# Kernel optimization log

Hardware: AMD Instinct MI355X
Metric: run time of the kernel (lower is better)

The kernel has to match this reference:

```python
import jax, jax.numpy as jnp
import numpy as np

B, N, M, DQ, DK, DV, H = 8, 1024, 1024, 512, 512, 512, 8
DS = DV // H  # dim_split = 64
NEG = -1e38


def _ln(x, g, b, eps=1e-5):
    mu = jnp.mean(x, -1, keepdims=True)
    var = jnp.mean((x - mu) ** 2, -1, keepdims=True)
    return (x - mu) * jax.lax.rsqrt(var + eps) * g + b


def setup_inputs() -> dict:
    key = jax.random.key(0)
    ks = jax.random.split(key, 16)
    s = 0.02
    return {
        "x": jax.random.normal(ks[0], (B, N, DQ), jnp.float32),
        "y": jax.random.normal(ks[1], (B, M, DK), jnp.float32),
        "x_mask": jax.random.randint(ks[2], (B, N), 0, 2).astype(bool),
        "y_mask": jax.random.randint(ks[3], (B, M), 0, 2).astype(bool),
        "Wq": jax.random.normal(ks[4], (DQ, DV), jnp.float32) * s,
        "Wk": jax.random.normal(ks[5], (DK, DV), jnp.float32) * s,
        "Wv": jax.random.normal(ks[6], (DK, DV), jnp.float32) * s,
        "Wo": jax.random.normal(ks[7], (DV, DQ), jnp.float32) * s,
        "W1": jax.random.normal(ks[8], (DQ, DQ), jnp.float32) * s,
        "b1": jnp.zeros((DQ,), jnp.float32),
        "W2": jax.random.normal(ks[9], (DQ, DQ), jnp.float32) * s,
        "b2": jnp.zeros((DQ,), jnp.float32),
        "g1": jnp.ones((DQ,), jnp.float32),
        "be1": jnp.zeros((DQ,), jnp.float32),
        "g2": jnp.ones((DQ,), jnp.float32),
        "be2": jnp.zeros((DQ,), jnp.float32),
    }


def reference(x, y, x_mask, y_mask, Wq, Wk, Wv, Wo, W1, b1, W2, b2, g1, be1, g2, be2):
    xm = x_mask[..., None]  # [B,N,1]
    ym = y_mask[..., None]  # [B,M,1]
    x = jnp.where(xm, 0.0, x)
    y = jnp.where(ym, 0.0, y)
    # projections (no bias); masked rows stay zero, re-mask as in source
    q = jnp.where(xm, 0.0, x @ Wq).reshape(B, N, H, DS)
    k = jnp.where(ym, 0.0, y @ Wk).reshape(B, M, H, DS)
    v = jnp.where(ym, 0.0, y @ Wv).reshape(B, M, H, DS)
    # scaled dot product; NOTE: scale is sqrt(dim_v), faithful to source
    sdp = jnp.einsum('bnhd,bmhd->bhnm', q, k) / np.sqrt(DV)
    mask = x_mask[:, None, :, None] | y_mask[:, None, None, :]  # [B,1,N,M]
    sdp = jnp.where(mask, NEG, sdp)
    alpha = jax.nn.softmax(sdp, axis=-1)  # softmax over keys (slot_att=False)
    att = jnp.einsum('bhnm,bmhd->bnhd', alpha, v).reshape(B, N, DV)
    att = jnp.where(xm, 0.0, att)
    o = x + att @ Wo
    o = _ln(o, g1, be1)
    ff = jax.nn.relu(o @ W1 + b1) @ W2 + b2
    o = _ln(o + ff, g2, be2)
    return jnp.where(xm, 0.0, o)
```

## Files before the change

kernel.cpp:

```cpp
#include <hip/hip_runtime.h>
#include <hip/hip_bf16.h>

typedef __bf16 bf16;
typedef __attribute__((ext_vector_type(4))) __bf16 bf16x4;
typedef __attribute__((ext_vector_type(8))) __bf16 bf16x8;
typedef __attribute__((ext_vector_type(4))) float f32x4;

#define B_ 8
#define N_ 1024
#define M_ 1024
#define H_ 8
#define ROWS_ (B_ * N_)

__device__ __forceinline__ f32x4 mfma16(bf16x8 a, bf16x8 b, f32x4 c) {
    return __builtin_amdgcn_mfma_f32_16x16x32_bf16(a, b, c, 0, 0, 0);
}

__device__ __forceinline__ void glds16(const void* g, void* l) {
    __builtin_amdgcn_global_load_lds((const __attribute__((address_space(1))) void*)g,
                                     (__attribute__((address_space(3))) void*)l, 16, 0, 0);
}

__global__ __launch_bounds__(256) void prep(const float* __restrict__ x, const float* __restrict__ y,
                                            bf16* __restrict__ Xb, bf16* __restrict__ Yb,
                                            const float* W0, const float* W1, const float* W2,
                                            const float* W3, const float* W4, const float* W5,
                                            bf16* T0, bf16* T1, bf16* T2, bf16* T3, bf16* T4, bf16* T5) {
    __shared__ float t[64][65];
    int bid = blockIdx.x;
    if (bid < 8192) {
        int i = bid * 256 + threadIdx.x;
        const float4* s;
        bf16x4* d;
        int j;
        if (i < 1048576) { s = (const float4*)x; d = (bf16x4*)Xb; j = i; }
        else             { s = (const float4*)y; d = (bf16x4*)Yb; j = i - 1048576; }
        float4 f = s[j];
        bf16x4 o = {(bf16)f.x, (bf16)f.y, (bf16)f.z, (bf16)f.w};
        d[j] = o;
        return;
    }
    int wb = bid - 8192;
    const float* srcs[6] = {W0, W1, W2, W3, W4, W5};
    bf16* dsts[6] = {T0, T1, T2, T3, T4, T5};
    const float* W = srcs[wb >> 6];
    bf16* Wt = dsts[wb >> 6];
    int tile = wb & 63;
    int k0 = (tile >> 3) * 64, n0 = (tile & 7) * 64;
    int tx = threadIdx.x & 63, ty = threadIdx.x >> 6;
#pragma unroll
    for (int j = 0; j < 16; ++j)
        t[ty + j * 4][tx] = W[(size_t)(k0 + ty + j * 4) * 512 + n0 + tx];
    __syncthreads();
#pragma unroll
    for (int j = 0; j < 16; ++j)
        Wt[(size_t)(n0 + ty + j * 4) * 512 + k0 + tx] = (bf16)t[tx][ty + j * 4];
}

__device__ __forceinline__ void gemm_core(const bf16* __restrict__ A, const bf16* __restrict__ Bt,
                                          int row0, int col0, bf16* As, bf16* Bs, f32x4 acc[4][4]) {
    int tid = threadIdx.x, wave = tid >> 6, lane = tid & 63;
    int lr = lane & 15, q4 = lane >> 4;
    const bf16 *Asrc[4], *Bsrc[4];
#pragma unroll
    for (int s = 0; s < 4; ++s) {
        int c = tid + s * 256, r = c >> 3, bk = (c & 7) ^ (r & 7);
        Asrc[s] = A + (size_t)(row0 + r) * 512 + bk * 8;
        Bsrc[s] = Bt + (size_t)(col0 + r) * 512 + bk * 8;
    }
    int wb = wave * 1024;
    int rbase = (wave & 1) * 64, cbase = (wave >> 1) * 64;
    for (int k0 = 0; k0 < 512; k0 += 64) {
        __syncthreads();
#pragma unroll
        for (int s = 0; s < 4; ++s) glds16(Asrc[s] + k0, (char*)As + s * 4096 + wb);
#pragma unroll
        for (int s = 0; s < 4; ++s) glds16(Bsrc[s] + k0, (char*)Bs + s * 4096 + wb);
        __syncthreads();
        bf16x8 af[4][2], bfr[4][2];
#pragma unroll
        for (int rt = 0; rt < 4; ++rt) {
            int row = rbase + rt * 16 + lr;
#pragma unroll
            for (int c = 0; c < 2; ++c)
                af[rt][c] = *(const bf16x8*)((const char*)As + (row * 8 + ((c * 4 + q4) ^ (row & 7))) * 16);
        }
#pragma unroll
        for (int ct = 0; ct < 4; ++ct) {
            int col = cbase + ct * 16 + lr;
#pragma unroll
            for (int c = 0; c < 2; ++c)
                bfr[ct][c] = *(const bf16x8*)((const char*)Bs + (col * 8 + ((c * 4 + q4) ^ (col & 7))) * 16);
        }
#pragma unroll
        for (int rt = 0; rt < 4; ++rt)
#pragma unroll
            for (int ct = 0; ct < 4; ++ct) {
                acc[rt][ct] = mfma16(af[rt][0], bfr[ct][0], acc[rt][ct]);
                acc[rt][ct] = mfma16(af[rt][1], bfr[ct][1], acc[rt][ct]);
            }
    }
}

__global__ __launch_bounds__(256, 2) void proj_qkv(const bf16* __restrict__ Xb, const bf16* __restrict__ Yb,
                                                   const bf16* __restrict__ Wqt, const bf16* __restrict__ Wkt,
                                                   const bf16* __restrict__ Wvt,
                                                   bf16* __restrict__ qb, bf16* __restrict__ kb,
                                                   bf16* __restrict__ Vt) {
    __shared__ bf16 As[128 * 64];
    __shared__ bf16 Bs[128 * 64];
    int z = blockIdx.z;
    const bf16 *A, *Bt;
    int row0, col0;
    if (z == 0)      { A = Xb;  Bt = Wqt; row0 = blockIdx.x * 128; col0 = blockIdx.y * 128; }
    else if (z == 1) { A = Yb;  Bt = Wkt; row0 = blockIdx.x * 128; col0 = blockIdx.y * 128; }
    else { A = Wvt; Bt = Yb; int flat = blockIdx.y * 64 + blockIdx.x; row0 = (flat & 3) * 128; col0 = (flat >> 2) * 128; }
    const f32x4 z4 = {0.f, 0.f, 0.f, 0.f};
    f32x4 acc[4][4];
#pragma unroll
    for (int rt = 0; rt < 4; ++rt)
#pragma unroll
        for (int ct = 0; ct < 4; ++ct) acc[rt][ct] = z4;
    gemm_core(A, Bt, row0, col0, As, Bs, acc);
    int wave = threadIdx.x >> 6, lane = threadIdx.x & 63, lr = lane & 15, q4 = lane >> 4;
    int rbase = (wave & 1) * 64, cbase = (wave >> 1) * 64;
    bf16* dst = (z == 0) ? qb : kb;
#pragma unroll
    for (int rt = 0; rt < 4; ++rt)
#pragma unroll
        for (int ct = 0; ct < 4; ++ct) {
            int col = col0 + cbase + ct * 16 + lr;
#pragma unroll
            for (int r = 0; r < 4; ++r) {
                int row = row0 + rbase + rt * 16 + q4 * 4 + r;
                bf16 v = (bf16)acc[rt][ct][r];
                if (z < 2) dst[(size_t)row * 512 + col] = v;
                else Vt[(size_t)((col >> 10) * 512 + row) * 1024 + (col & 1023)] = v;
            }
        }
}

template <int MODE>
__global__ __launch_bounds__(256, 2) void gemm_bt(const bf16* __restrict__ A, const bf16* __restrict__ Bt,
                                                  const float* __restrict__ bias, void* __restrict__ Cout) {
    __shared__ bf16 As[128 * 64];
    __shared__ bf16 Bs[128 * 64];
    int row0 = blockIdx.x * 128, col0 = blockIdx.y * 128;
    const f32x4 z4 = {0.f, 0.f, 0.f, 0.f};
    f32x4 acc[4][4];
#pragma unroll
    for (int rt = 0; rt < 4; ++rt)
#pragma unroll
        for (int ct = 0; ct < 4; ++ct) acc[rt][ct] = z4;
    gemm_core(A, Bt, row0, col0, As, Bs, acc);
    int wave = threadIdx.x >> 6, lane = threadIdx.x & 63, lr = lane & 15, q4 = lane >> 4;
    int rbase = (wave & 1) * 64, cbase = (wave >> 1) * 64;
#pragma unroll
    for (int rt = 0; rt < 4; ++rt)
#pragma unroll
        for (int ct = 0; ct < 4; ++ct) {
            int col = col0 + cbase + ct * 16 + lr;
            float bv = (MODE >= 2) ? bias[col] : 0.0f;
#pragma unroll
            for (int r = 0; r < 4; ++r) {
                int row = row0 + rbase + rt * 16 + q4 * 4 + r;
                float v = acc[rt][ct][r] + bv;
                if (MODE == 3) v = fmaxf(v, 0.0f);
                if (MODE == 3) ((bf16*)Cout)[(size_t)row * 512 + col] = (bf16)v;
                else           ((float*)Cout)[(size_t)row * 512 + col] = v;
            }
        }
}

__global__ __launch_bounds__(256, 2) void attn(const bf16* __restrict__ Q, const bf16* __restrict__ Kb,
                                               const bf16* __restrict__ Vt, const int* __restrict__ ymask,
                                               bf16* __restrict__ att) {
    __shared__ bf16 Ks[64 * 64];
    __shared__ bf16 Vs[64 * 64];
    __shared__ bf16 Ps[4][32 * 72];

    int bid = blockIdx.x;
    int bh = bid & 63, n0 = (bid >> 6) * 128;
    int b = bh >> 3, h = bh & 7;
    int tid = threadIdx.x, wave = tid >> 6, lane = tid & 63;
    int lr = lane & 15, q4 = lane >> 4;
    const float scale = 0.044194173824159216f;

    bf16x8 aq[2][2];
#pragma unroll
    for (int rt = 0; rt < 2; ++rt) {
        const bf16* qp = Q + (size_t)((b << 10) + n0 + wave * 32 + rt * 16 + lr) * 512 + h * 64 + q4 * 8;
        aq[rt][0] = *(const bf16x8*)qp;
        aq[rt][1] = *(const bf16x8*)(qp + 32);
    }

    const bf16 *Ksrc[2], *Vsrc[2];
#pragma unroll
    for (int s = 0; s < 2; ++s) {
        int c = tid + s * 256, r = c >> 3, bk = (c & 7) ^ (r & 7);
        Ksrc[s] = Kb + (size_t)((b << 10) + r) * 512 + h * 64 + bk * 8;
        Vsrc[s] = Vt + (size_t)(b * 512 + h * 64 + r) * 1024 + bk * 8;
    }
    int wb = wave * 1024;

    const f32x4 zv = {0.f, 0.f, 0.f, 0.f};
    f32x4 O[2][4];
    float lsum[2][4];
#pragma unroll
    for (int rt = 0; rt < 2; ++rt) {
#pragma unroll
        for (int dt = 0; dt < 4; ++dt) O[rt][dt] = zv;
#pragma unroll
        for (int rr = 0; rr < 4; ++rr) lsum[rt][rr] = 0.f;
    }

    for (int m0 = 0; m0 < M_; m0 += 64) {
        int mk = ymask[(b << 10) + m0 + lane];
        __syncthreads();
#pragma unroll
        for (int s = 0; s < 2; ++s) {
            glds16(Ksrc[s] + (size_t)m0 * 512, (char*)Ks + s * 4096 + wb);
            glds16(Vsrc[s] + m0, (char*)Vs + s * 4096 + wb);
        }
        __syncthreads();

#pragma unroll
        for (int nt = 0; nt < 4; ++nt) {
            int krow = nt * 16 + lr;
            bf16x8 kf0 = *(const bf16x8*)((const char*)Ks + (krow * 8 + (q4 ^ (krow & 7))) * 16);
            bf16x8 kf1 = *(const bf16x8*)((const char*)Ks + (krow * 8 + ((4 + q4) ^ (krow & 7))) * 16);
            int mkv = __shfl(mk, krow);
#pragma unroll
            for (int rt = 0; rt < 2; ++rt) {
                f32x4 s = mfma16(aq[rt][0], kf0, zv);
                s = mfma16(aq[rt][1], kf1, s);
#pragma unroll
                for (int rr = 0; rr < 4; ++rr) {
                    float p = mkv ? 0.0f : __expf(s[rr] * scale);
                    lsum[rt][rr] += p;
                    Ps[wave][(rt * 16 + q4 * 4 + rr) * 72 + krow] = (bf16)p;
                }
            }
        }
        bf16x8 ap[2][2];
#pragma unroll
        for (int rt = 0; rt < 2; ++rt) {
            ap[rt][0] = *(const bf16x8*)&Ps[wave][(rt * 16 + lr) * 72 + q4 * 8];
            ap[rt][1] = *(const bf16x8*)&Ps[wave][(rt * 16 + lr) * 72 + 32 + q4 * 8];
        }
#pragma unroll
        for (int dt = 0; dt < 4; ++dt) {
            int vrow = dt * 16 + lr;
            bf16x8 vf0 = *(const bf16x8*)((const char*)Vs + (vrow * 8 + (q4 ^ (vrow & 7))) * 16);
            bf16x8 vf1 = *(const bf16x8*)((const char*)Vs + (vrow * 8 + ((4 + q4) ^ (vrow & 7))) * 16);
#pragma unroll
            for (int rt = 0; rt < 2; ++rt) {
                O[rt][dt] = mfma16(ap[rt][0], vf0, O[rt][dt]);
                O[rt][dt] = mfma16(ap[rt][1], vf1, O[rt][dt]);
            }
        }
    }

#pragma unroll
    for (int rt = 0; rt < 2; ++rt)
#pragma unroll
        for (int rr = 0; rr < 4; ++rr) {
            float v = lsum[rt][rr];
            v += __shfl_xor(v, 1); v += __shfl_xor(v, 2);
            v += __shfl_xor(v, 4); v += __shfl_xor(v, 8);
            lsum[rt][rr] = (v > 0.0f) ? (1.0f / v) : 0.0f;
        }
#pragma unroll
    for (int rt = 0; rt < 2; ++rt)
#pragma unroll
        for (int dt = 0; dt < 4; ++dt)
#pragma unroll
            for (int rr = 0; rr < 4; ++rr) {
                int row = n0 + wave * 32 + rt * 16 + q4 * 4 + rr;
                att[(size_t)((b << 10) + row) * 512 + h * 64 + dt * 16 + lr] =
                    (bf16)(O[rt][dt][rr] * lsum[rt][rr]);
            }
}

__global__ __launch_bounds__(128) void ln1_k(const float* __restrict__ X, const float* __restrict__ R,
                                             const float* __restrict__ g, const float* __restrict__ be,
                                             float* __restrict__ O, bf16* __restrict__ Obf) {
    int row = blockIdx.x, t = threadIdx.x;
    float4 xv = ((const float4*)(X + (size_t)row * 512))[t];
    float4 rv = ((const float4*)(R + (size_t)row * 512))[t];
    float4 o = {xv.x + rv.x, xv.y + rv.y, xv.z + rv.z, xv.w + rv.w};
    float s = o.x + o.y + o.z + o.w;
    float sq = o.x * o.x + o.y * o.y + o.z * o.z + o.w * o.w;
#pragma unroll
    for (int off = 1; off < 64; off <<= 1) { s += __shfl_xor(s, off); sq += __shfl_xor(sq, off); }
    __shared__ float ls[2], lq[2];
    if ((t & 63) == 0) { ls[t >> 6] = s; lq[t >> 6] = sq; }
    __syncthreads();
    s = ls[0] + ls[1]; sq = lq[0] + lq[1];
    float mu = s * (1.0f / 512.0f);
    float var = sq * (1.0f / 512.0f) - mu * mu;
    float rs = rsqrtf(var + 1e-5f);
    float4 gv = ((const float4*)g)[t];
    float4 bv = ((const float4*)be)[t];
    float4 r4 = {(o.x - mu) * rs * gv.x + bv.x, (o.y - mu) * rs * gv.y + bv.y,
                 (o.z - mu) * rs * gv.z + bv.z, (o.w - mu) * rs * gv.w + bv.w};
    ((float4*)(O + (size_t)row * 512))[t] = r4;
    bf16x4 b4 = {(bf16)r4.x, (bf16)r4.y, (bf16)r4.z, (bf16)r4.w};
    ((bf16x4*)(Obf + (size_t)row * 512))[t] = b4;
}

__global__ __launch_bounds__(128) void ln2_k(const float* __restrict__ O, const float* __restrict__ F,
                                             const float* __restrict__ g, const float* __restrict__ be,
                                             const int* __restrict__ xmask, float* __restrict__ out) {
    int row = blockIdx.x, t = threadIdx.x;
    float4 xv = ((const float4*)(O + (size_t)row * 512))[t];
    float4 rv = ((const float4*)(F + (size_t)row * 512))[t];
    float4 o = {xv.x + rv.x, xv.y + rv.y, xv.z + rv.z, xv.w + rv.w};
    float s = o.x + o.y + o.z + o.w;
    float sq = o.x * o.x + o.y * o.y + o.z * o.z + o.w * o.w;
#pragma unroll
    for (int off = 1; off < 64; off <<= 1) { s += __shfl_xor(s, off); sq += __shfl_xor(sq, off); }
    __shared__ float ls[2], lq[2];
    if ((t & 63) == 0) { ls[t >> 6] = s; lq[t >> 6] = sq; }
    __syncthreads();
    s = ls[0] + ls[1]; sq = lq[0] + lq[1];
    float mu = s * (1.0f / 512.0f);
    float var = sq * (1.0f / 512.0f) - mu * mu;
    float rs = rsqrtf(var + 1e-5f);
    int msk = xmask[row];
    float4 gv = ((const float4*)g)[t];
    float4 bv = ((const float4*)be)[t];
    float4 r4 = {(o.x - mu) * rs * gv.x + bv.x, (o.y - mu) * rs * gv.y + bv.y,
                 (o.z - mu) * rs * gv.z + bv.z, (o.w - mu) * rs * gv.w + bv.w};
    if (msk) r4 = {0.f, 0.f, 0.f, 0.f};
    ((float4*)(out + (size_t)row * 512))[t] = r4;
}

extern "C" void kernel_launch(void* const* d_in, const int* in_sizes, int n_in,
                              void* d_out, int out_size, void* d_ws, size_t ws_size,
                              hipStream_t stream) {
    const float* x   = (const float*)d_in[0];
    const float* y   = (const float*)d_in[1];
    const int*   xm  = (const int*)d_in[2];
    const int*   ym  = (const int*)d_in[3];
    const float* Wq  = (const float*)d_in[4];
    const float* Wk  = (const float*)d_in[5];
    const float* Wv  = (const float*)d_in[6];
    const float* Wo  = (const float*)d_in[7];
    const float* W1  = (const float*)d_in[8];
    const float* b1  = (const float*)d_in[9];
    const float* W2  = (const float*)d_in[10];
    const float* b2  = (const float*)d_in[11];
    const float* g1  = (const float*)d_in[12];
    const float* be1 = (const float*)d_in[13];
    const float* g2  = (const float*)d_in[14];
    const float* be2 = (const float*)d_in[15];

    char* ws = (char*)d_ws;
    const size_t WT_SZ  = 512 * 512 * sizeof(bf16);
    const size_t XB_SZ  = (size_t)ROWS_ * 512 * sizeof(bf16);
    const size_t F32_SZ = (size_t)ROWS_ * 512 * sizeof(float);

    bf16* Wqt = (bf16*)(ws + 0 * WT_SZ);
    bf16* Wkt = (bf16*)(ws + 1 * WT_SZ);
    bf16* Wvt = (bf16*)(ws + 2 * WT_SZ);
    bf16* Wot = (bf16*)(ws + 3 * WT_SZ);
    bf16* W1t = (bf16*)(ws + 4 * WT_SZ);
    bf16* W2t = (bf16*)(ws + 5 * WT_SZ);
    size_t off = 6 * WT_SZ;
    bf16* Xb  = (bf16*)(ws + off); off += XB_SZ;
    bf16* Yb  = (bf16*)(ws + off); off += XB_SZ;
    bf16* qb  = (bf16*)(ws + off); off += XB_SZ;
    bf16* kb  = (bf16*)(ws + off); off += XB_SZ;
    bf16* Vt  = (bf16*)(ws + off); off += XB_SZ;
    float* awo = (float*)(ws + off); off += F32_SZ;
    float* ob  = (float*)(ws + off); off += F32_SZ;
    bf16* attb = Xb;
    bf16* obf  = qb;
    bf16* hb   = Yb;
    float* fb  = awo;

    prep<<<8576, 256, 0, stream>>>(x, y, Xb, Yb, Wq, Wk, Wv, Wo, W1, W2,
                                   Wqt, Wkt, Wvt, Wot, W1t, W2t);

    proj_qkv<<<dim3(64, 4, 3), 256, 0, stream>>>(Xb, Yb, Wqt, Wkt, Wvt, qb, kb, Vt);

    attn<<<512, 256, 0, stream>>>(qb, kb, Vt, ym, attb);

    dim3 gg(64, 4);
    gemm_bt<0><<<gg, 256, 0, stream>>>(attb, Wot, nullptr, awo);
    ln1_k<<<ROWS_, 128, 0, stream>>>(x, awo, g1, be1, ob, obf);
    gemm_bt<3><<<gg, 256, 0, stream>>>(obf, W1t, b1, hb);
    gemm_bt<2><<<gg, 256, 0, stream>>>(hb, W2t, b2, fb);
    ln2_k<<<ROWS_, 128, 0, stream>>>(ob, fb, g2, be2, xm, (float*)d_out);
}
```

Measured before the change: 221.3 us.

## Double-buffer LDS in GEMM and attention kernels, shrink GEMM tiles to 128x64

The shared GEMM core now double-buffers its LDS tiles, issuing the next k-slice's global-to-LDS loads before computing on the current one, with one barrier per iteration instead of two. The tile shrinks from 128x128 to 128x64, which doubles the grid so there are more blocks to fill the GPU. The attention kernel also double-buffers its K/V tiles and replaces the masked branch with an additive -1e30 bias inside the exponent. The intent is to hide global load latency and raise parallelism, at the cost of more LDS per block and more redundant A-tile loads.

```diff
diff --git a/kernel.cpp b/kernel.cpp
--- a/kernel.cpp
+++ b/kernel.cpp
@@ -58,42 +58,56 @@
 }
 
 __device__ __forceinline__ void gemm_core(const bf16* __restrict__ A, const bf16* __restrict__ Bt,
-                                          int row0, int col0, bf16* As, bf16* Bs, f32x4 acc[4][4]) {
+                                          int row0, int col0, char* AsB, char* BsB, f32x4 acc[2][4]) {
     int tid = threadIdx.x, wave = tid >> 6, lane = tid & 63;
     int lr = lane & 15, q4 = lane >> 4;
-    const bf16 *Asrc[4], *Bsrc[4];
+    const bf16 *Asrc[4], *Bsrc[2];
 #pragma unroll
     for (int s = 0; s < 4; ++s) {
         int c = tid + s * 256, r = c >> 3, bk = (c & 7) ^ (r & 7);
         Asrc[s] = A + (size_t)(row0 + r) * 512 + bk * 8;
+    }
+#pragma unroll
+    for (int s = 0; s < 2; ++s) {
+        int c = tid + s * 256, r = c >> 3, bk = (c & 7) ^ (r & 7);
         Bsrc[s] = Bt + (size_t)(col0 + r) * 512 + bk * 8;
     }
     int wb = wave * 1024;
-    int rbase = (wave & 1) * 64, cbase = (wave >> 1) * 64;
-    for (int k0 = 0; k0 < 512; k0 += 64) {
+#pragma unroll
+    for (int s = 0; s < 4; ++s) glds16(Asrc[s], AsB + s * 4096 + wb);
+#pragma unroll
+    for (int s = 0; s < 2; ++s) glds16(Bsrc[s], BsB + s * 4096 + wb);
+#pragma unroll
+    for (int it = 0; it < 8; ++it) {
         __syncthreads();
-#pragma unroll
-        for (int s = 0; s < 4; ++s) glds16(Asrc[s] + k0, (char*)As + s * 4096 + wb);
-#pragma unroll
-        for (int s = 0; s < 4; ++s) glds16(Bsrc[s] + k0, (char*)Bs + s * 4096 + wb);
-        __syncthreads();
-        bf16x8 af[4][2], bfr[4][2];
-#pragma unroll
-        for (int rt = 0; rt < 4; ++rt) {
-            int row = rbase + rt * 16 + lr;
+        const char* Ac = AsB + (it & 1) * 16384;
+        const char* Bc = BsB + (it & 1) * 8192;
+        if (it < 7) {
+            char* An = AsB + ((it + 1) & 1) * 16384;
+            char* Bn = BsB + ((it + 1) & 1) * 8192;
+            int k0 = (it + 1) * 64;
+#pragma unroll
+            for (int s = 0; s < 4; ++s) glds16(Asrc[s] + k0, An + s * 4096 + wb);
+#pragma unroll
+            for (int s = 0; s < 2; ++s) glds16(Bsrc[s] + k0, Bn + s * 4096 + wb);
+        }
+        bf16x8 af[2][2], bfr[4][2];
+#pragma unroll
+        for (int rt = 0; rt < 2; ++rt) {
+            int row = wave * 32 + rt * 16 + lr;
 #pragma unroll
             for (int c = 0; c < 2; ++c)
-                af[rt][c] = *(const bf16x8*)((const char*)As + (row * 8 + ((c * 4 + q4) ^ (row & 7))) * 16);
+                af[rt][c] = *(const bf16x8*)(Ac + (row * 8 + ((c * 4 + q4) ^ (row & 7))) * 16);
         }
 #pragma unroll
         for (int ct = 0; ct < 4; ++ct) {
-            int col = cbase + ct * 16 + lr;
+            int col = ct * 16 + lr;
 #pragma unroll
             for (int c = 0; c < 2; ++c)
-                bfr[ct][c] = *(const bf16x8*)((const char*)Bs + (col * 8 + ((c * 4 + q4) ^ (col & 7))) * 16);
-        }
-#pragma unroll
-        for (int rt = 0; rt < 4; ++rt)
+                bfr[ct][c] = *(const bf16x8*)(Bc + (col * 8 + ((c * 4 + q4) ^ (col & 7))) * 16);
+        }
+#pragma unroll
+        for (int rt = 0; rt < 2; ++rt)
 #pragma unroll
             for (int ct = 0; ct < 4; ++ct) {
                 acc[rt][ct] = mfma16(af[rt][0], bfr[ct][0], acc[rt][ct]);
@@ -107,32 +121,27 @@
                                                    const bf16* __restrict__ Wvt,
                                                    bf16* __restrict__ qb, bf16* __restrict__ kb,
                                                    bf16* __restrict__ Vt) {
-    __shared__ bf16 As[128 * 64];
-    __shared__ bf16 Bs[128 * 64];
+    __shared__ char AsB[2 * 16384];
+    __shared__ char BsB[2 * 8192];
     int z = blockIdx.z;
     const bf16 *A, *Bt;
     int row0, col0;
-    if (z == 0)      { A = Xb;  Bt = Wqt; row0 = blockIdx.x * 128; col0 = blockIdx.y * 128; }
-    else if (z == 1) { A = Yb;  Bt = Wkt; row0 = blockIdx.x * 128; col0 = blockIdx.y * 128; }
-    else { A = Wvt; Bt = Yb; int flat = blockIdx.y * 64 + blockIdx.x; row0 = (flat & 3) * 128; col0 = (flat >> 2) * 128; }
+    if (z == 0)      { A = Xb;  Bt = Wqt; row0 = blockIdx.x * 128; col0 = blockIdx.y * 64; }
+    else if (z == 1) { A = Yb;  Bt = Wkt; row0 = blockIdx.x * 128; col0 = blockIdx.y * 64; }
+    else { A = Wvt; Bt = Yb; int flat = blockIdx.y * 64 + blockIdx.x; row0 = (flat & 3) * 128; col0 = (flat >> 2) * 64; }
     const f32x4 z4 = {0.f, 0.f, 0.f, 0.f};
-    f32x4 acc[4][4];
-#pragma unroll
-    for (int rt = 0; rt < 4; ++rt)
-#pragma unroll
-        for (int ct = 0; ct < 4; ++ct) acc[rt][ct] = z4;
-    gemm_core(A, Bt, row0, col0, As, Bs, acc);
+    f32x4 acc[2][4] = {{z4, z4, z4, z4}, {z4, z4, z4, z4}};
+    gemm_core(A, Bt, row0, col0, AsB, BsB, acc);
     int wave = threadIdx.x >> 6, lane = threadIdx.x & 63, lr = lane & 15, q4 = lane >> 4;
-    int rbase = (wave & 1) * 64, cbase = (wave >> 1) * 64;
     bf16* dst = (z == 0) ? qb : kb;
 #pragma unroll
-    for (int rt = 0; rt < 4; ++rt)
+    for (int rt = 0; rt < 2; ++rt)
 #pragma unroll
         for (int ct = 0; ct < 4; ++ct) {
-            int col = col0 + cbase + ct * 16 + lr;
+            int col = col0 + ct * 16 + lr;
 #pragma unroll
             for (int r = 0; r < 4; ++r) {
-                int row = row0 + rbase + rt * 16 + q4 * 4 + r;
+                int row = row0 + wave * 32 + rt * 16 + q4 * 4 + r;
                 bf16 v = (bf16)acc[rt][ct][r];
                 if (z < 2) dst[(size_t)row * 512 + col] = v;
                 else Vt[(size_t)((col >> 10) * 512 + row) * 1024 + (col & 1023)] = v;
@@ -143,27 +152,22 @@
 template <int MODE>
 __global__ __launch_bounds__(256, 2) void gemm_bt(const bf16* __restrict__ A, const bf16* __restrict__ Bt,
                                                   const float* __restrict__ bias, void* __restrict__ Cout) {
-    __shared__ bf16 As[128 * 64];
-    __shared__ bf16 Bs[128 * 64];
-    int row0 = blockIdx.x * 128, col0 = blockIdx.y * 128;
+    __shared__ char AsB[2 * 16384];
+    __shared__ char BsB[2 * 8192];
+    int row0 = blockIdx.x * 128, col0 = blockIdx.y * 64;
     const f32x4 z4 = {0.f, 0.f, 0.f, 0.f};
-    f32x4 acc[4][4];
-#pragma unroll
-    for (int rt = 0; rt < 4; ++rt)
-#pragma unroll
-        for (int ct = 0; ct < 4; ++ct) acc[rt][ct] = z4;
-    gemm_core(A, Bt, row0, col0, As, Bs, acc);
+    f32x4 acc[2][4] = {{z4, z4, z4, z4}, {z4, z4, z4, z4}};
+    gemm_core(A, Bt, row0, col0, AsB, BsB, acc);
     int wave = threadIdx.x >> 6, lane = threadIdx.x & 63, lr = lane & 15, q4 = lane >> 4;
-    int rbase = (wave & 1) * 64, cbase = (wave >> 1) * 64;
-#pragma unroll
-    for (int rt = 0; rt < 4; ++rt)
+#pragma unroll
+    for (int rt = 0; rt < 2; ++rt)
 #pragma unroll
         for (int ct = 0; ct < 4; ++ct) {
-            int col = col0 + cbase + ct * 16 + lr;
+            int col = col0 + ct * 16 + lr;
             float bv = (MODE >= 2) ? bias[col] : 0.0f;
 #pragma unroll
             for (int r = 0; r < 4; ++r) {
-                int row = row0 + rbase + rt * 16 + q4 * 4 + r;
+                int row = row0 + wave * 32 + rt * 16 + q4 * 4 + r;
                 float v = acc[rt][ct][r] + bv;
                 if (MODE == 3) v = fmaxf(v, 0.0f);
                 if (MODE == 3) ((bf16*)Cout)[(size_t)row * 512 + col] = (bf16)v;
@@ -175,8 +179,8 @@
 __global__ __launch_bounds__(256, 2) void attn(const bf16* __restrict__ Q, const bf16* __restrict__ Kb,
                                                const bf16* __restrict__ Vt, const int* __restrict__ ymask,
                                                bf16* __restrict__ att) {
-    __shared__ bf16 Ks[64 * 64];
-    __shared__ bf16 Vs[64 * 64];
+    __shared__ bf16 Ks[2][64 * 64];
+    __shared__ bf16 Vs[2][64 * 64];
     __shared__ bf16 Ps[4][32 * 72];
 
     int bid = blockIdx.x;
@@ -202,6 +206,7 @@
         Vsrc[s] = Vt + (size_t)(b * 512 + h * 64 + r) * 1024 + bk * 8;
     }
     int wb = wave * 1024;
+    const int* ymb = ymask + (b << 10);
 
     const f32x4 zv = {0.f, 0.f, 0.f, 0.f};
     f32x4 O[2][4];
@@ -214,29 +219,41 @@
         for (int rr = 0; rr < 4; ++rr) lsum[rt][rr] = 0.f;
     }
 
-    for (int m0 = 0; m0 < M_; m0 += 64) {
-        int mk = ymask[(b << 10) + m0 + lane];
+#pragma unroll
+    for (int s = 0; s < 2; ++s) {
+        glds16(Ksrc[s], (char*)Ks[0] + s * 4096 + wb);
+        glds16(Vsrc[s], (char*)Vs[0] + s * 4096 + wb);
+    }
+
+    for (int it = 0; it < 16; ++it) {
         __syncthreads();
-#pragma unroll
-        for (int s = 0; s < 2; ++s) {
-            glds16(Ksrc[s] + (size_t)m0 * 512, (char*)Ks + s * 4096 + wb);
-            glds16(Vsrc[s] + m0, (char*)Vs + s * 4096 + wb);
-        }
-        __syncthreads();
+        const char* K_ = (const char*)Ks[it & 1];
+        const char* V_ = (const char*)Vs[it & 1];
+        if (it < 15) {
+            char* Kn = (char*)Ks[(it + 1) & 1];
+            char* Vn = (char*)Vs[(it + 1) & 1];
+            size_t m1 = (size_t)(it + 1) * 64;
+#pragma unroll
+            for (int s = 0; s < 2; ++s) {
+                glds16(Ksrc[s] + m1 * 512, Kn + s * 4096 + wb);
+                glds16(Vsrc[s] + m1, Vn + s * 4096 + wb);
+            }
+        }
+        int m0 = it * 64;
 
 #pragma unroll
         for (int nt = 0; nt < 4; ++nt) {
             int krow = nt * 16 + lr;
-            bf16x8 kf0 = *(const bf16x8*)((const char*)Ks + (krow * 8 + (q4 ^ (krow & 7))) * 16);
-            bf16x8 kf1 = *(const bf16x8*)((const char*)Ks + (krow * 8 + ((4 + q4) ^ (krow & 7))) * 16);
-            int mkv = __shfl(mk, krow);
+            bf16x8 kf0 = *(const bf16x8*)(K_ + (krow * 8 + (q4 ^ (krow & 7))) * 16);
+            bf16x8 kf1 = *(const bf16x8*)(K_ + (krow * 8 + ((4 + q4) ^ (krow & 7))) * 16);
+            float fm = ymb[m0 + krow] ? -1e30f : 0.0f;
 #pragma unroll
             for (int rt = 0; rt < 2; ++rt) {
                 f32x4 s = mfma16(aq[rt][0], kf0, zv);
                 s = mfma16(aq[rt][1], kf1, s);
 #pragma unroll
                 for (int rr = 0; rr < 4; ++rr) {
-                    float p = mkv ? 0.0f : __expf(s[rr] * scale);
+                    float p = __expf(fmaf(s[rr], scale, fm));
                     lsum[rt][rr] += p;
                     Ps[wave][(rt * 16 + q4 * 4 + rr) * 72 + krow] = (bf16)p;
                 }
@@ -251,8 +268,8 @@
 #pragma unroll
         for (int dt = 0; dt < 4; ++dt) {
             int vrow = dt * 16 + lr;
-            bf16x8 vf0 = *(const bf16x8*)((const char*)Vs + (vrow * 8 + (q4 ^ (vrow & 7))) * 16);
-            bf16x8 vf1 = *(const bf16x8*)((const char*)Vs + (vrow * 8 + ((4 + q4) ^ (vrow & 7))) * 16);
+            bf16x8 vf0 = *(const bf16x8*)(V_ + (vrow * 8 + (q4 ^ (vrow & 7))) * 16);
+            bf16x8 vf1 = *(const bf16x8*)(V_ + (vrow * 8 + ((4 + q4) ^ (vrow & 7))) * 16);
 #pragma unroll
             for (int rt = 0; rt < 2; ++rt) {
                 O[rt][dt] = mfma16(ap[rt][0], vf0, O[rt][dt]);
@@ -383,11 +400,11 @@
     prep<<<8576, 256, 0, stream>>>(x, y, Xb, Yb, Wq, Wk, Wv, Wo, W1, W2,
                                    Wqt, Wkt, Wvt, Wot, W1t, W2t);
 
-    proj_qkv<<<dim3(64, 4, 3), 256, 0, stream>>>(Xb, Yb, Wqt, Wkt, Wvt, qb, kb, Vt);
+    proj_qkv<<<dim3(64, 8, 3), 256, 0, stream>>>(Xb, Yb, Wqt, Wkt, Wvt, qb, kb, Vt);
 
     attn<<<512, 256, 0, stream>>>(qb, kb, Vt, ym, attb);
 
-    dim3 gg(64, 4);
+    dim3 gg(64, 8);
     gemm_bt<0><<<gg, 256, 0, stream>>>(attb, Wot, nullptr, awo);
     ln1_k<<<ROWS_, 128, 0, stream>>>(x, awo, g1, be1, ob, obf);
     gemm_bt<3><<<gg, 256, 0, stream>>>(obf, W1t, b1, hb);
```

Result: no change. 219.6 us (-0.7%).
